# Kernel tuning notes

Hardware: AMD Instinct MI355X
Metric: run time of the kernel (lower is better)

Reference implementation:

```python
import jax, jax.numpy as jnp
import numpy as np

B, S, D, FF, E, K = 32, 32, 768, 3072, 8, 2


def setup_inputs() -> dict:
    key = jax.random.key(0)
    ks = jax.random.split(key, 6)
    rn = lambda k, shape, sc: (jax.random.normal(k, shape, dtype=jnp.float32) * sc)
    return {
        "x": rn(ks[0], (B, S, D), 1.0),
        "attention_mask": jnp.ones((B, S), dtype=jnp.float32),
        "Wg": rn(ks[1], (D, E), 0.02),          # gate Linear weight
        "bg": jnp.zeros((E,), jnp.float32),      # gate Linear bias
        "W1": rn(ks[2], (E, D, FF), 0.02),       # per-expert FFN up-proj
        "b1": jnp.zeros((E, FF), jnp.float32),
        "W2": rn(ks[3], (E, FF, D), 0.02),       # per-expert FFN down-proj
        "b2": jnp.zeros((E, D), jnp.float32),
    }


def reference(x, attention_mask, Wg, bg, W1, b1, W2, b2):
    # --- sentence-level gating (source overwrites mask with ones) ---
    mask = jnp.ones_like(attention_mask)                      # [B,S]
    x_avg = (x * mask[..., None]).sum(1) / mask[..., None].sum(1)  # [B,D]
    logits_gate = x_avg @ Wg + bg                             # [B,E]
    prob_gate = jax.nn.softmax(logits_gate, axis=-1)
    select_prob_gate, gate = jax.lax.top_k(prob_gate, K)      # [B,K], [B,K]

    # --- per-expert FFN on all sentences (dense equivalent of the
    #     sort/split/vstack dispatch in the source) ---
    # h: [E,B,S,FF]
    h = jnp.einsum('bsd,edf->ebsf', x, W1) + b1[:, None, None, :]
    h = jax.nn.gelu(h, approximate=False)
    out = jnp.einsum('ebsf,efd->ebsd', h, W2) + b2[:, None, None, :]  # [E,B,S,D]

    # --- combine: the source sums the topk expert outputs UNWEIGHTED
    #     (tmp_prob is computed but never applied) ---
    sel = jax.nn.one_hot(gate, E, dtype=x.dtype).sum(1)       # [B,E], entries in {0,1}
    moe_result = jnp.einsum('be,ebsd->bsd', sel, out)         # [B,S,D]

    return moe_result, select_prob_gate, gate
```

## Files before the change

### kernel.cpp

```cpp
#include <hip/hip_runtime.h>
#include <hip/hip_bf16.h>
#include <math.h>

#define BB 32
#define SS 32
#define DD 768
#define FFD 3072
#define EE 8
#define KK 2
#define NPAIR 64
#define MAXT 22

typedef __attribute__((ext_vector_type(8))) short short8;
typedef __attribute__((ext_vector_type(4))) float f32x4;
typedef __attribute__((ext_vector_type(8))) unsigned short us8;


#define H_OFF    4096
#define XBF_OFF  (H_OFF + 12582912)
#define PART_OFF (XBF_OFF + 1572864)
#define PZ       (2048 * 768)
#define WS_MAIN  ((size_t)PART_OFF + 2ull * PZ * 2ull)

__device__ __forceinline__ unsigned short f2bf(float f) {
    __hip_bfloat16 h = __float2bfloat16(f);
    return __builtin_bit_cast(unsigned short, h);
}
__device__ __forceinline__ float bf2f(unsigned short u) {
    __hip_bfloat16 h = __builtin_bit_cast(__hip_bfloat16, u);
    return __bfloat162float(h);
}

__device__ __forceinline__ int lds_off(int row, int byte_in_row) {
    return row * 128 + (byte_in_row ^ ((row & 7) << 4));
}

__global__ __launch_bounds__(256) void gate_kernel(
    const float* __restrict__ x, const float* __restrict__ Wg,
    const float* __restrict__ bg, float* __restrict__ out,
    int* __restrict__ gates)
{
    int b = blockIdx.x;
    int tid = threadIdx.x;

    float acc[EE];
#pragma unroll
    for (int e = 0; e < EE; ++e) acc[e] = 0.f;

    for (int d = tid; d < DD; d += 256) {
        float xs = 0.f;
        const float* xp = x + (size_t)b * SS * DD + d;
#pragma unroll
        for (int s = 0; s < SS; ++s) xs += xp[(size_t)s * DD];
#pragma unroll
        for (int e = 0; e < EE; ++e) acc[e] += xs * Wg[d * EE + e];
    }

    __shared__ float red[EE][256];
#pragma unroll
    for (int e = 0; e < EE; ++e) red[e][tid] = acc[e];
    __syncthreads();
    for (int off = 128; off > 0; off >>= 1) {
        if (tid < off) {
#pragma unroll
            for (int e = 0; e < EE; ++e) red[e][tid] += red[e][tid + off];
        }
        __syncthreads();
    }

    if (tid == 0) {
        float lg[EE], p[EE];
        float m = -1e30f;
#pragma unroll
        for (int e = 0; e < EE; ++e) {
            lg[e] = red[e][0] / (float)SS + bg[e];
            m = fmaxf(m, lg[e]);
        }
        float sum = 0.f;
#pragma unroll
        for (int e = 0; e < EE; ++e) { p[e] = expf(lg[e] - m); sum += p[e]; }
        float inv = 1.f / sum;
#pragma unroll
        for (int e = 0; e < EE; ++e) p[e] *= inv;

        int i1 = 0;
        for (int e = 1; e < EE; ++e) if (p[e] > p[i1]) i1 = e;
        int i2 = (i1 == 0) ? 1 : 0;
        for (int e = 0; e < EE; ++e) if (e != i1 && p[e] > p[i2]) i2 = e;

        float* prob_out = out + (size_t)BB * SS * DD;
        float* gate_out = prob_out + BB * KK;
        prob_out[b * KK + 0] = p[i1];
        prob_out[b * KK + 1] = p[i2];
        gate_out[b * KK + 0] = (float)i1;
        gate_out[b * KK + 1] = (float)i2;
        gates[b * KK + 0] = i1;
        gates[b * KK + 1] = i2;
    }
}

__global__ void sched_kernel(int* __restrict__ wsi)
{
    if (threadIdx.x != 0 || blockIdx.x != 0) return;
    const int* gates = wsi;
    int* spair = wsi + 64;
    int* te_e = wsi + 128;
    int* te_s = wsi + 152;
    int* te_n = wsi + 176;
    int* slotof = wsi + 200;

    int cnt[EE];
    for (int e = 0; e < EE; ++e) cnt[e] = 0;
    for (int p = 0; p < NPAIR; ++p) cnt[gates[p]]++;
    int start[EE + 1];
    start[0] = 0;
    for (int e = 0; e < EE; ++e) start[e + 1] = start[e] + cnt[e];
    int fill[EE];
    for (int e = 0; e < EE; ++e) fill[e] = start[e];
    for (int p = 0; p < NPAIR; ++p) {
        int s = fill[gates[p]]++;
        spair[s] = p;
        slotof[p] = s;
    }

    int t = 0;
    for (int e = 0; e < EE; ++e) {
        for (int o = 0; o < cnt[e]; o += 4) {
            te_e[t] = e;
            te_s[t] = start[e] + o;
            te_n[t] = (cnt[e] - o) < 4 ? (cnt[e] - o) : 4;
            ++t;
        }
    }
    for (; t < MAXT; ++t) te_n[t] = 0;
}

__global__ __launch_bounds__(256) void pack_x(
    const float* __restrict__ x, unsigned short* __restrict__ xbf)
{
    int i = blockIdx.x * 256 + threadIdx.x;
    const float4* src = (const float4*)(x + (size_t)i * 8);
    float4 v0 = src[0], v1 = src[1];
    us8 u;
    u[0] = f2bf(v0.x); u[1] = f2bf(v0.y); u[2] = f2bf(v0.z); u[3] = f2bf(v0.w);
    u[4] = f2bf(v1.x); u[5] = f2bf(v1.y); u[6] = f2bf(v1.z); u[7] = f2bf(v1.w);
    *(us8*)(xbf + (size_t)i * 8) = u;
}

__global__ __launch_bounds__(256) void init_kernel(
    const int* __restrict__ gates, const float* __restrict__ b2,
    float* __restrict__ out)
{
    int idx = blockIdx.x * 256 + threadIdx.x;
    if (idx >= BB * SS * DD) return;
    int b = idx / (SS * DD);
    int d = idx % DD;
    int e0 = gates[b * KK + 0];
    int e1 = gates[b * KK + 1];
    out[idx] = b2[e0 * DD + d] + b2[e1 * DD + d];
}

__global__ __launch_bounds__(256, 2) void up_gemm(
    const unsigned short* __restrict__ xbf, const float* __restrict__ W1,
    const float* __restrict__ b1, const int* __restrict__ wsi,
    unsigned short* __restrict__ H)
{
    int tile = blockIdx.y;
    int np = wsi[176 + tile];
    if (np == 0) return;
    int e = wsi[128 + tile];
    int slot0 = wsi[152 + tile];
    int nt = blockIdx.x;
    int tid = threadIdx.x;
    int wid = tid >> 6, lane = tid & 63;
    int wm = wid >> 1, wn = wid & 1;

    __shared__ char lds[65536];

    const unsigned short* asrc[4];
    int aoff[4];
#pragma unroll
    for (int i = 0; i < 4; ++i) {
        int c = tid + i * 256;
        int row = c >> 3, ch = c & 7;
        int lp = row >> 5;
        int lpc = lp < np ? lp : np - 1;
        int pair = wsi[64 + slot0 + lpc];
        int b = pair >> 1;
        asrc[i] = xbf + ((size_t)(b * SS + (row & 31))) * DD + ch * 8;
        aoff[i] = lds_off(row, ch * 16);
    }
    int n = tid & 127, kq = tid >> 7;
    const float* bsrc = W1 + ((size_t)e * DD + kq * 32) * FFD + nt * 128 + n;
    int boff[4];
#pragma unroll
    for (int m4 = 0; m4 < 4; ++m4) boff[m4] = lds_off(n, kq * 64 + m4 * 16);

    f32x4 acc[4][4];
#pragma unroll
    for (int i = 0; i < 4; ++i)
#pragma unroll
        for (int j = 0; j < 4; ++j) acc[i][j] = (f32x4)0.f;

    float brg[32];
    us8 arg[4];

    auto issue = [&](int k0) {
        const float* wp = bsrc + (size_t)k0 * FFD;
#pragma unroll
        for (int j = 0; j < 32; ++j) brg[j] = wp[(size_t)j * FFD];
#pragma unroll
        for (int i = 0; i < 4; ++i) arg[i] = *(const us8*)(asrc[i] + k0);
    };
    auto store = [&](int p) {
        char* Al = lds + p * 32768;
        char* Bl = Al + 16384;
#pragma unroll
        for (int i = 0; i < 4; ++i) *(us8*)(Al + aoff[i]) = arg[i];
#pragma unroll
        for (int m4 = 0; m4 < 4; ++m4) {
            us8 u;
#pragma unroll
            for (int m = 0; m < 8; ++m) u[m] = f2bf(brg[m4 * 8 + m]);
            *(us8*)(Bl + boff[m4]) = u;
        }
    };
    auto compute = [&](int p) {
        char* Al = lds + p * 32768;
        char* Bl = Al + 16384;
#pragma unroll
        for (int kk = 0; kk < 2; ++kk) {
            int kb = kk * 64 + (lane >> 4) * 16;
            short8 af[4], bf[4];
#pragma unroll
            for (int mf = 0; mf < 4; ++mf)
                af[mf] = *(short8*)(Al + lds_off(wm * 64 + mf * 16 + (lane & 15), kb));
#pragma unroll
            for (int nf = 0; nf < 4; ++nf)
                bf[nf] = *(short8*)(Bl + lds_off(wn * 64 + nf * 16 + (lane & 15), kb));
#pragma unroll
            for (int mf = 0; mf < 4; ++mf)
#pragma unroll
                for (int nf = 0; nf < 4; ++nf)
                    acc[mf][nf] = __builtin_amdgcn_mfma_f32_16x16x32_bf16(
                        af[mf], bf[nf], acc[mf][nf], 0, 0, 0);
        }
    };

    const int steps = 12;
    issue(0);
    store(0);
    issue(64);
    __syncthreads();
#pragma unroll 2
    for (int s = 0; s < steps; ++s) {
        int p = s & 1;
        compute(p);
        if (s < steps - 1) {
            store(p ^ 1);
            if (s < steps - 2) issue((s + 2) * 64);
        }
        __syncthreads();
    }

    float bias[4];
#pragma unroll
    for (int nf = 0; nf < 4; ++nf)
        bias[nf] = b1[e * FFD + nt * 128 + wn * 64 + nf * 16 + (lane & 15)];
#pragma unroll
    for (int mf = 0; mf < 4; ++mf) {
#pragma unroll
        for (int i = 0; i < 4; ++i) {
            int row = wm * 64 + mf * 16 + (lane >> 4) * 4 + i;
            if ((row >> 5) >= np) continue;
            size_t srow = (size_t)(slot0 * 32 + row);
#pragma unroll
            for (int nf = 0; nf < 4; ++nf) {
                int f = nt * 128 + wn * 64 + nf * 16 + (lane & 15);
                float h = acc[mf][nf][i] + bias[nf];
                float g = 0.5f * h * (1.0f + erff(h * 0.70710678118654752f));
                H[srow * FFD + f] = f2bf(g);
            }
        }
    }
}

template<int MODE>
__global__ __launch_bounds__(256, 2) void down_gemm(
    const unsigned short* __restrict__ H, const float* __restrict__ W2,
    const int* __restrict__ wsi, unsigned short* __restrict__ part,
    float* __restrict__ out)
{
    int tile = blockIdx.y;
    int np = wsi[176 + tile];
    if (np == 0) return;
    int e = wsi[128 + tile];
    int slot0 = wsi[152 + tile];
    int nt = blockIdx.x;
    int z = blockIdx.z;
    int zb = z * (FFD / 2);
    int tid = threadIdx.x;
    int wid = tid >> 6, lane = tid & 63;
    int wm = wid >> 1, wn = wid & 1;

    __shared__ char lds[65536];

    const unsigned short* asrc[4];
    int aoff[4];
#pragma unroll
    for (int i = 0; i < 4; ++i) {
        int c = tid + i * 256;
        int row = c >> 3, ch = c & 7;
        int rc = row < np * 32 ? row : np * 32 - 1;
        asrc[i] = H + (size_t)(slot0 * 32 + rc) * FFD + zb + ch * 8;
        aoff[i] = lds_off(row, ch * 16);
    }
    int n = tid & 127, kq = tid >> 7;
    const float* bsrc = W2 + ((size_t)e * FFD + zb + kq * 32) * DD + nt * 128 + n;
    int boff[4];
#pragma unroll
    for (int m4 = 0; m4 < 4; ++m4) boff[m4] = lds_off(n, kq * 64 + m4 * 16);

    f32x4 acc[4][4];
#pragma unroll
    for (int i = 0; i < 4; ++i)
#pragma unroll
        for (int j = 0; j < 4; ++j) acc[i][j] = (f32x4)0.f;

    float brg[32];
    us8 arg[4];

    auto issue = [&](int k0) {
        const float* wp = bsrc + (size_t)k0 * DD;
#pragma unroll
        for (int j = 0; j < 32; ++j) brg[j] = wp[(size_t)j * DD];
#pragma unroll
        for (int i = 0; i < 4; ++i) arg[i] = *(const us8*)(asrc[i] + k0);
    };
    auto store = [&](int p) {
        char* Al = lds + p * 32768;
        char* Bl = Al + 16384;
#pragma unroll
        for (int i = 0; i < 4; ++i) *(us8*)(Al + aoff[i]) = arg[i];
#pragma unroll
        for (int m4 = 0; m4 < 4; ++m4) {
            us8 u;
#pragma unroll
            for (int m = 0; m < 8; ++m) u[m] = f2bf(brg[m4 * 8 + m]);
            *(us8*)(Bl + boff[m4]) = u;
        }
    };
    auto compute = [&](int p) {
        char* Al = lds + p * 32768;
        char* Bl = Al + 16384;
#pragma unroll
        for (int kk = 0; kk < 2; ++kk) {
            int kb = kk * 64 + (lane >> 4) * 16;
            short8 af[4], bf[4];
#pragma unroll
            for (int mf = 0; mf < 4; ++mf)
                af[mf] = *(short8*)(Al + lds_off(wm * 64 + mf * 16 + (lane & 15), kb));
#pragma unroll
            for (int nf = 0; nf < 4; ++nf)
                bf[nf] = *(short8*)(Bl + lds_off(wn * 64 + nf * 16 + (lane & 15), kb));
#pragma unroll
            for (int mf = 0; mf < 4; ++mf)
#pragma unroll
                for (int nf = 0; nf < 4; ++nf)
                    acc[mf][nf] = __builtin_amdgcn_mfma_f32_16x16x32_bf16(
                        af[mf], bf[nf], acc[mf][nf], 0, 0, 0);
        }
    };

    const int steps = 24;
    issue(0);
    store(0);
    issue(64);
    __syncthreads();
#pragma unroll 2
    for (int s = 0; s < steps; ++s) {
        int p = s & 1;
        compute(p);
        if (s < steps - 1) {
            store(p ^ 1);
            if (s < steps - 2) issue((s + 2) * 64);
        }
        __syncthreads();
    }

#pragma unroll
    for (int mf = 0; mf < 4; ++mf) {
#pragma unroll
        for (int i = 0; i < 4; ++i) {
            int row = wm * 64 + mf * 16 + (lane >> 4) * 4 + i;
            int lp = row >> 5;
            if (lp >= np) continue;
            int col = nt * 128 + wn * 64 + (lane & 15);
            if (MODE == 0) {
                size_t srow = (size_t)(slot0 * 32 + row);
                unsigned short* pp = part + (size_t)z * PZ + srow * DD + col;
#pragma unroll
                for (int nf = 0; nf < 4; ++nf) pp[nf * 16] = f2bf(acc[mf][nf][i]);
            } else {
                int pair = wsi[64 + slot0 + lp];
                int b = pair >> 1;
                int sI = row & 31;
                float* op = out + ((size_t)(b * SS + sI)) * DD + col;
#pragma unroll
                for (int nf = 0; nf < 4; ++nf)
                    atomicAdd(op + nf * 16, acc[mf][nf][i]);
            }
        }
    }
}

__global__ __launch_bounds__(512) void reduce_kernel(
    const unsigned short* __restrict__ part, const int* __restrict__ wsi,
    const float* __restrict__ b2, float* __restrict__ out)
{
    int i8 = blockIdx.x * 512 + threadIdx.x;
    int flat = i8 * 8;
    int b = flat / (SS * DD);
    int r = flat - b * (SS * DD);
    int s = r / DD;
    int d = r - s * DD;

    int e0 = wsi[b * KK + 0];
    int e1 = wsi[b * KK + 1];
    int sl0 = wsi[200 + b * KK + 0];
    int sl1 = wsi[200 + b * KK + 1];
    size_t r0 = (size_t)(sl0 * 32 + s) * DD + d;
    size_t r1 = (size_t)(sl1 * 32 + s) * DD + d;

    us8 p00 = *(const us8*)(part + r0);
    us8 p01 = *(const us8*)(part + PZ + r0);
    us8 p10 = *(const us8*)(part + r1);
    us8 p11 = *(const us8*)(part + PZ + r1);
    const float* bb0 = b2 + e0 * DD + d;
    const float* bb1 = b2 + e1 * DD + d;

    float v[8];
#pragma unroll
    for (int j = 0; j < 8; ++j)
        v[j] = bf2f(p00[j]) + bf2f(p01[j]) + bf2f(p10[j]) + bf2f(p11[j])
             + bb0[j] + bb1[j];
    float4* op = (float4*)(out + flat);
    op[0] = make_float4(v[0], v[1], v[2], v[3]);
    op[1] = make_float4(v[4], v[5], v[6], v[7]);
}

extern "C" void kernel_launch(void* const* d_in, const int* in_sizes, int n_in,
                              void* d_out, int out_size, void* d_ws, size_t ws_size,
                              hipStream_t stream) {
    const float* x  = (const float*)d_in[0];
    const float* Wg = (const float*)d_in[2];
    const float* bg = (const float*)d_in[3];
    const float* W1 = (const float*)d_in[4];
    const float* b1 = (const float*)d_in[5];
    const float* W2 = (const float*)d_in[6];
    const float* b2 = (const float*)d_in[7];
    float* out = (float*)d_out;

    int* wsi = (int*)d_ws;
    unsigned short* H    = (unsigned short*)((char*)d_ws + H_OFF);
    unsigned short* xbf  = (unsigned short*)((char*)d_ws + XBF_OFF);
    unsigned short* part = (unsigned short*)((char*)d_ws + PART_OFF);

    gate_kernel<<<BB, 256, 0, stream>>>(x, Wg, bg, out, wsi);
    sched_kernel<<<1, 64, 0, stream>>>(wsi);
    pack_x<<<(BB * SS * DD) / (256 * 8), 256, 0, stream>>>(x, xbf);
    up_gemm<<<dim3(FFD / 128, MAXT), 256, 0, stream>>>(xbf, W1, b1, wsi, H);

    if (ws_size >= WS_MAIN) {
        down_gemm<0><<<dim3(DD / 128, MAXT, 2), 256, 0, stream>>>(
            H, W2, wsi, part, out);
        reduce_kernel<<<(BB * SS * DD) / (512 * 8), 512, 0, stream>>>(
            part, wsi, b2, out);
    } else {
        init_kernel<<<(BB * SS * DD + 255) / 256, 256, 0, stream>>>(wsi, b2, out);
        down_gemm<1><<<dim3(DD / 128, MAXT, 2), 256, 0, stream>>>(
            H, W2, wsi, part, out);
    }
}
```

Measured before the change: 102.0 us.

## Deepen register prefetch pipeline and split down-GEMM K four ways

Both expert GEMMs now use two register staging buffers, so global loads for step s+2 are issued while step s computes, instead of a single buffer that was stored right before the next issue. The down-projection splits the FF reduction into four chunks instead of two, doubling the grid to give more blocks for parallelism. The reduce kernel then sums four bf16 partial sums per expert. The partial buffer is moved to overlap the xbf region, which is no longer needed by that point. This raises register pressure and partial-sum traffic, and adds extra bf16 rounding of the partials.

New measurement: 110.3 us. 8.1% more time.

```diff
diff --git a/kernel.cpp b/kernel.cpp
--- a/kernel.cpp
+++ b/kernel.cpp
@@ -18,9 +18,9 @@
 
 #define H_OFF    4096
 #define XBF_OFF  (H_OFF + 12582912)
-#define PART_OFF (XBF_OFF + 1572864)
+#define PART_OFF XBF_OFF
 #define PZ       (2048 * 768)
-#define WS_MAIN  ((size_t)PART_OFF + 2ull * PZ * 2ull)
+#define WS_MAIN  ((size_t)PART_OFF + 4ull * PZ * 2ull)
 
 __device__ __forceinline__ unsigned short f2bf(float f) {
     __hip_bfloat16 h = __float2bfloat16(f);
@@ -202,26 +202,26 @@
 #pragma unroll
         for (int j = 0; j < 4; ++j) acc[i][j] = (f32x4)0.f;
 
-    float brg[32];
-    us8 arg[4];
-
-    auto issue = [&](int k0) {
+    float bB0[32], bB1[32];
+    us8 bA0[4], bA1[4];
+
+    auto issue = [&](int k0, float (&bB)[32], us8 (&bA)[4]) {
         const float* wp = bsrc + (size_t)k0 * FFD;
 #pragma unroll
-        for (int j = 0; j < 32; ++j) brg[j] = wp[(size_t)j * FFD];
-#pragma unroll
-        for (int i = 0; i < 4; ++i) arg[i] = *(const us8*)(asrc[i] + k0);
-    };
-    auto store = [&](int p) {
+        for (int j = 0; j < 32; ++j) bB[j] = wp[(size_t)j * FFD];
+#pragma unroll
+        for (int i = 0; i < 4; ++i) bA[i] = *(const us8*)(asrc[i] + k0);
+    };
+    auto store = [&](int p, const float (&bB)[32], const us8 (&bA)[4]) {
         char* Al = lds + p * 32768;
         char* Bl = Al + 16384;
 #pragma unroll
-        for (int i = 0; i < 4; ++i) *(us8*)(Al + aoff[i]) = arg[i];
+        for (int i = 0; i < 4; ++i) *(us8*)(Al + aoff[i]) = bA[i];
 #pragma unroll
         for (int m4 = 0; m4 < 4; ++m4) {
             us8 u;
 #pragma unroll
-            for (int m = 0; m < 8; ++m) u[m] = f2bf(brg[m4 * 8 + m]);
+            for (int m = 0; m < 8; ++m) u[m] = f2bf(bB[m4 * 8 + m]);
             *(us8*)(Bl + boff[m4]) = u;
         }
     };
@@ -248,17 +248,19 @@
     };
 
     const int steps = 12;
-    issue(0);
-    store(0);
-    issue(64);
+    issue(0, bB0, bA0);
+    issue(64, bB1, bA1);
+    store(0, bB0, bA0);
     __syncthreads();
-#pragma unroll 2
-    for (int s = 0; s < steps; ++s) {
-        int p = s & 1;
-        compute(p);
-        if (s < steps - 1) {
-            store(p ^ 1);
-            if (s < steps - 2) issue((s + 2) * 64);
+    for (int s = 0; s < steps; s += 2) {
+        compute(0);
+        if (s + 2 < steps) issue((s + 2) * 64, bB0, bA0);
+        store(1, bB1, bA1);
+        __syncthreads();
+        compute(1);
+        if (s + 2 < steps) {
+            if (s + 3 < steps) issue((s + 3) * 64, bB1, bA1);
+            store(0, bB0, bA0);
         }
         __syncthreads();
     }
@@ -298,7 +300,7 @@
     int slot0 = wsi[152 + tile];
     int nt = blockIdx.x;
     int z = blockIdx.z;
-    int zb = z * (FFD / 2);
+    int zb = z * (FFD / 4);
     int tid = threadIdx.x;
     int wid = tid >> 6, lane = tid & 63;
     int wm = wid >> 1, wn = wid & 1;
@@ -327,26 +329,26 @@
 #pragma unroll
         for (int j = 0; j < 4; ++j) acc[i][j] = (f32x4)0.f;
 
-    float brg[32];
-    us8 arg[4];
-
-    auto issue = [&](int k0) {
+    float bB0[32], bB1[32];
+    us8 bA0[4], bA1[4];
+
+    auto issue = [&](int k0, float (&bB)[32], us8 (&bA)[4]) {
         const float* wp = bsrc + (size_t)k0 * DD;
 #pragma unroll
-        for (int j = 0; j < 32; ++j) brg[j] = wp[(size_t)j * DD];
-#pragma unroll
-        for (int i = 0; i < 4; ++i) arg[i] = *(const us8*)(asrc[i] + k0);
-    };
-    auto store = [&](int p) {
+        for (int j = 0; j < 32; ++j) bB[j] = wp[(size_t)j * DD];
+#pragma unroll
+        for (int i = 0; i < 4; ++i) bA[i] = *(const us8*)(asrc[i] + k0);
+    };
+    auto store = [&](int p, const float (&bB)[32], const us8 (&bA)[4]) {
         char* Al = lds + p * 32768;
         char* Bl = Al + 16384;
 #pragma unroll
-        for (int i = 0; i < 4; ++i) *(us8*)(Al + aoff[i]) = arg[i];
+        for (int i = 0; i < 4; ++i) *(us8*)(Al + aoff[i]) = bA[i];
 #pragma unroll
         for (int m4 = 0; m4 < 4; ++m4) {
             us8 u;
 #pragma unroll
-            for (int m = 0; m < 8; ++m) u[m] = f2bf(brg[m4 * 8 + m]);
+            for (int m = 0; m < 8; ++m) u[m] = f2bf(bB[m4 * 8 + m]);
             *(us8*)(Bl + boff[m4]) = u;
         }
     };
@@ -372,18 +374,20 @@
         }
     };
 
-    const int steps = 24;
-    issue(0);
-    store(0);
-    issue(64);
+    const int steps = 12;
+    issue(0, bB0, bA0);
+    issue(64, bB1, bA1);
+    store(0, bB0, bA0);
     __syncthreads();
-#pragma unroll 2
-    for (int s = 0; s < steps; ++s) {
-        int p = s & 1;
-        compute(p);
-        if (s < steps - 1) {
-            store(p ^ 1);
-            if (s < steps - 2) issue((s + 2) * 64);
+    for (int s = 0; s < steps; s += 2) {
+        compute(0);
+        if (s + 2 < steps) issue((s + 2) * 64, bB0, bA0);
+        store(1, bB1, bA1);
+        __syncthreads();
+        compute(1);
+        if (s + 2 < steps) {
+            if (s + 3 < steps) issue((s + 3) * 64, bB1, bA1);
+            store(0, bB0, bA0);
         }
         __syncthreads();
     }
@@ -432,18 +436,19 @@
     size_t r0 = (size_t)(sl0 * 32 + s) * DD + d;
     size_t r1 = (size_t)(sl1 * 32 + s) * DD + d;
 
-    us8 p00 = *(const us8*)(part + r0);
-    us8 p01 = *(const us8*)(part + PZ + r0);
-    us8 p10 = *(const us8*)(part + r1);
-    us8 p11 = *(const us8*)(part + PZ + r1);
     const float* bb0 = b2 + e0 * DD + d;
     const float* bb1 = b2 + e1 * DD + d;
 
     float v[8];
 #pragma unroll
-    for (int j = 0; j < 8; ++j)
-        v[j] = bf2f(p00[j]) + bf2f(p01[j]) + bf2f(p10[j]) + bf2f(p11[j])
-             + bb0[j] + bb1[j];
+    for (int j = 0; j < 8; ++j) v[j] = bb0[j] + bb1[j];
+#pragma unroll
+    for (int z = 0; z < 4; ++z) {
+        us8 p0 = *(const us8*)(part + (size_t)z * PZ + r0);
+        us8 p1 = *(const us8*)(part + (size_t)z * PZ + r1);
+#pragma unroll
+        for (int j = 0; j < 8; ++j) v[j] += bf2f(p0[j]) + bf2f(p1[j]);
+    }
     float4* op = (float4*)(out + flat);
     op[0] = make_float4(v[0], v[1], v[2], v[3]);
     op[1] = make_float4(v[4], v[5], v[6], v[7]);
@@ -472,13 +477,13 @@
     up_gemm<<<dim3(FFD / 128, MAXT), 256, 0, stream>>>(xbf, W1, b1, wsi, H);
 
     if (ws_size >= WS_MAIN) {
-        down_gemm<0><<<dim3(DD / 128, MAXT, 2), 256, 0, stream>>>(
+        down_gemm<0><<<dim3(DD / 128, MAXT, 4), 256, 0, stream>>>(
             H, W2, wsi, part, out);
         reduce_kernel<<<(BB * SS * DD) / (512 * 8), 512, 0, stream>>>(
             part, wsi, b2, out);
     } else {
         init_kernel<<<(BB * SS * DD + 255) / 256, 256, 0, stream>>>(wsi, b2, out);
-        down_gemm<1><<<dim3(DD / 128, MAXT, 2), 256, 0, stream>>>(
+        down_gemm<1><<<dim3(DD / 128, MAXT, 4), 256, 0, stream>>>(
             H, W2, wsi, part, out);
     }
 }
```
